# Performance work log

Measured on AMD Instinct MI355X. Metric: run time of the kernel, lower is better.

The kernel has to match this reference:

```python
import jax, jax.numpy as jnp
import numpy as np

N1 = 4096
N2 = 4096


def _encoder(x, w1, b1, w2, b2, w3, b3):
    # fc1 -> fc2 -> fc3 -> relu (relu only after fc3, matching the torch code)
    h = x @ w1.T + b1
    h = h @ w2.T + b2
    h = h @ w3.T + b3
    return jax.nn.relu(h)


def _self_attention(x, adj, alpha, W):
    # tmp_i = sum_j [adj_ij==1] * alpha_ij * W * x_j ; tmp_i /= deg_i ; tmp_i += x_i (only if deg_i != 0)
    a = (adj == 1).astype(x.dtype)          # [N, N]
    deg = a.sum(axis=1)                     # [N]
    agg = (a * alpha) @ x                   # [N, 64] masked weighted aggregation
    agg = agg * W[0, 0]
    safe_deg = jnp.maximum(deg, 1.0)
    out = agg / safe_deg[:, None] + x       # residual
    return jnp.where((deg != 0.0)[:, None], out, jnp.zeros_like(out))


def setup_inputs() -> dict:
    key = jax.random.key(0)
    ks = jax.random.split(key, 20)
    s = 0.02  # weight scale to keep activations sane through the 4096->256->128->64 MLP
    inp = {
        "x1": jax.random.normal(ks[0], (N1, N1), jnp.float32),
        "x2": jax.random.normal(ks[1], (N2, N2), jnp.float32),
        "adj1": jax.random.randint(ks[2], (N1, N1), 0, 2, jnp.int32),
        "adj2": jax.random.randint(ks[3], (N2, N2), 0, 2, jnp.int32),
        "e1_w1": jax.random.normal(ks[4], (256, N1), jnp.float32) * s,
        "e1_b1": jnp.zeros((256,), jnp.float32),
        "e1_w2": jax.random.normal(ks[5], (128, 256), jnp.float32) * s,
        "e1_b2": jnp.zeros((128,), jnp.float32),
        "e1_w3": jax.random.normal(ks[6], (64, 128), jnp.float32) * s,
        "e1_b3": jnp.zeros((64,), jnp.float32),
        "e2_w1": jax.random.normal(ks[7], (256, N2), jnp.float32) * s,
        "e2_b1": jnp.zeros((256,), jnp.float32),
        "e2_w2": jax.random.normal(ks[8], (128, 256), jnp.float32) * s,
        "e2_b2": jnp.zeros((128,), jnp.float32),
        "e2_w3": jax.random.normal(ks[9], (64, 128), jnp.float32) * s,
        "e2_b3": jnp.zeros((64,), jnp.float32),
        "W": jax.random.normal(ks[10], (1, 1), jnp.float32),
        "alpha1": jax.random.normal(ks[11], (N1, N1), jnp.float32),
        "clf_w": jax.random.normal(ks[12], (2, (N1 + N2) * 64), jnp.float32) * s,
        "clf_b": jnp.zeros((2,), jnp.float32),
    }
    return inp


def reference(x1, x2, adj1, adj2,
              e1_w1, e1_b1, e1_w2, e1_b2, e1_w3, e1_b3,
              e2_w1, e2_b1, e2_w2, e2_b2, e2_w3, e2_b3,
              W, alpha1, clf_w, clf_b):
    h1 = _encoder(x1, e1_w1, e1_b1, e1_w2, e1_b2, e1_w3, e1_b3)  # [N1, 64]
    h2 = _encoder(x2, e2_w1, e2_b1, e2_w2, e2_b2, e2_w3, e2_b3)  # [N2, 64]
    # NOTE: original torch code uses self.alpha1 for BOTH graphs (alpha2 is unused)
    new1 = _self_attention(h1, adj1, alpha1, W)
    new2 = _self_attention(h2, adj2, alpha1[:N2, :N2], W)
    feat = jnp.concatenate([new1, new2], axis=0).reshape(1, -1)  # [1, (N1+N2)*64]
    return feat @ clf_w.T + clf_b  # [1, 2]
```

## Files before the change

kernel.cpp:

```cpp
#include <hip/hip_runtime.h>
#include <hip/hip_bf16.h>
#include <stdint.h>

#define N 4096

typedef __attribute__((ext_vector_type(4))) float f32x4;
typedef __attribute__((ext_vector_type(8))) short s16x8;

__device__ inline unsigned short f2bf(float f) {
    unsigned int u = __float_as_uint(f);
    u += 0x7fffu + ((u >> 16) & 1u);
    return (unsigned short)(u >> 16);
}
__device__ inline float bf2f(unsigned short h) {
    return __uint_as_float(((unsigned int)h) << 16);
}

__global__ void k0a(const float* __restrict__ w2a, const float* __restrict__ w3a,
                    const float* __restrict__ b1a, const float* __restrict__ b2a, const float* __restrict__ b3a,
                    const float* __restrict__ w2b, const float* __restrict__ w3b,
                    const float* __restrict__ b1b, const float* __restrict__ b2b, const float* __restrict__ b3b,
                    float* __restrict__ T, float* __restrict__ beff) {
    const int g  = blockIdx.x >> 5;
    const int nb = blockIdx.x & 31;
    const float* w2 = g ? w2b : w2a;
    const float* w3 = g ? w3b : w3a;
    const int c  = threadIdx.x;
    const int n0 = nb * 2;
    float a0 = 0.f, a1 = 0.f;
#pragma unroll 8
    for (int r = 0; r < 128; ++r) {
        float w = w2[r * 256 + c];
        a0 += w3[n0 * 128 + r] * w;
        a1 += w3[n0 * 128 + 128 + r] * w;
    }
    float* Tg = T + g * 64 * 256;
    Tg[n0 * 256 + c]       = a0;
    Tg[(n0 + 1) * 256 + c] = a1;

    if (nb == 0) {
        __shared__ float ps[256];
        __shared__ float u[128];
        const float* b1 = g ? b1b : b1a;
        const float* b2 = g ? b2b : b2a;
        const float* b3 = g ? b3b : b3a;
        {
            const int r = threadIdx.x >> 1, half = threadIdx.x & 1;
            float s = 0.f;
#pragma unroll 8
            for (int cc = 0; cc < 128; ++cc) s += w2[r * 256 + half * 128 + cc] * b1[half * 128 + cc];
            ps[threadIdx.x] = s;
        }
        __syncthreads();
        if (threadIdx.x < 128)
            u[threadIdx.x] = ps[2 * threadIdx.x] + ps[2 * threadIdx.x + 1] + b2[threadIdx.x];
        __syncthreads();
        {
            const int n = threadIdx.x >> 2, qr = threadIdx.x & 3;
            float s = 0.f;
#pragma unroll
            for (int r = 0; r < 32; ++r) s += w3[n * 128 + qr * 32 + r] * u[qr * 32 + r];
            ps[threadIdx.x] = s;
        }
        __syncthreads();
        if (threadIdx.x < 64)
            beff[g * 64 + threadIdx.x] = ps[4 * threadIdx.x] + ps[4 * threadIdx.x + 1]
                                       + ps[4 * threadIdx.x + 2] + ps[4 * threadIdx.x + 3] + b3[threadIdx.x];
    }
}

__global__ __launch_bounds__(256) void k0b(const float* __restrict__ w1a, const float* __restrict__ w1b,
                                           const float* __restrict__ T,
                                           unsigned short* __restrict__ Wfrag) {
    const int b  = blockIdx.x;
    const int g = b >> 8, n4 = (b >> 4) & 15, kchunk = b & 15;
    const float* w1 = g ? w1b : w1a;
    const int kx = kchunk * 256 + threadIdx.x;
    const float* Tg = T + (size_t)(g * 64 + n4 * 4) * 256;
    float acc[4] = {0.f, 0.f, 0.f, 0.f};
#pragma unroll 8
    for (int r = 0; r < 256; ++r) {
        float w = w1[(size_t)r * N + kx];
#pragma unroll
        for (int j = 0; j < 4; ++j) acc[j] += Tg[j * 256 + r] * w;
    }
    const int kc = kx >> 6, cc = (kx >> 5) & 1, q = (kx >> 3) & 3, ko = kx & 7;
#pragma unroll
    for (int j = 0; j < 4; ++j) {
        const int n = n4 * 4 + j;
        const int ng = n >> 4, l15 = n & 15;
        const int lane = q * 16 + l15;
        const unsigned short hi = f2bf(acc[j]);
        const unsigned short lo = f2bf(acc[j] - bf2f(hi));
        const size_t unit = ((((size_t)g * 64 + kc) * 4 + ng) * 2 + cc) * 2;
        Wfrag[unit * 512 + lane * 8 + ko]       = hi;
        Wfrag[(unit + 1) * 512 + lane * 8 + ko] = lo;
    }
}

__global__ __launch_bounds__(512, 2) void k1(const float* __restrict__ x1, const float* __restrict__ x2,
                                             const unsigned short* __restrict__ Wfrag,
                                             float* __restrict__ ph) {
    const int b  = blockIdx.x;
    const int rt = b >> 2, ks = b & 3;
    const int g  = rt >> 6;
    const int rbase = (rt & 63) * 64;
    const float* x = g ? x2 : x1;

    const int t = threadIdx.x;
    const int lane = t & 63, w = t >> 6;
    const int rg = w & 3, kh = w >> 2;
    const int q = lane >> 4, l15 = lane & 15;

    __shared__ float accs_h[4][4][64][4];

    f32x4 acc[4];
#pragma unroll
    for (int ng = 0; ng < 4; ++ng) acc[ng] = (f32x4){0.f, 0.f, 0.f, 0.f};

    const float* xrow = x + (size_t)(rbase + rg * 16 + l15) * N;
    const int kcbase = ks * 16 + kh * 8;

    float4 pa0, pa1, ra0, ra1;
    s16x8 pbh[4], pbl[4], rbh[4], rbl[4];

#define K1_LOAD(A0, A1, BH, BL, IT) do { \
        const int kc_ = kcbase + ((IT) >> 1), c_ = (IT) & 1; \
        const int ka_ = kc_ * 64 + c_ * 32 + q * 8; \
        A0 = *(const float4*)&xrow[ka_]; \
        A1 = *(const float4*)&xrow[ka_ + 4]; \
        _Pragma("unroll") \
        for (int ng = 0; ng < 4; ++ng) { \
            const size_t unit = ((((size_t)g * 64 + kc_) * 4 + ng) * 2 + c_) * 2; \
            BH[ng] = *(const s16x8*)&Wfrag[unit * 512 + lane * 8]; \
            BL[ng] = *(const s16x8*)&Wfrag[(unit + 1) * 512 + lane * 8]; \
        } \
    } while (0)

#define K1_COMP(A0, A1, BH, BL) do { \
        float xv[8] = {A0.x, A0.y, A0.z, A0.w, A1.x, A1.y, A1.z, A1.w}; \
        s16x8 ah, al; \
        _Pragma("unroll") \
        for (int j = 0; j < 8; ++j) { \
            unsigned short hh = f2bf(xv[j]); \
            ah[j] = (short)hh; \
            al[j] = (short)f2bf(xv[j] - bf2f(hh)); \
        } \
        _Pragma("unroll") \
        for (int ng = 0; ng < 4; ++ng) { \
            acc[ng] = __builtin_amdgcn_mfma_f32_16x16x32_bf16(al, BH[ng], acc[ng], 0, 0, 0); \
            acc[ng] = __builtin_amdgcn_mfma_f32_16x16x32_bf16(ah, BL[ng], acc[ng], 0, 0, 0); \
            acc[ng] = __builtin_amdgcn_mfma_f32_16x16x32_bf16(ah, BH[ng], acc[ng], 0, 0, 0); \
        } \
    } while (0)

    K1_LOAD(pa0, pa1, pbh, pbl, 0);
#pragma unroll
    for (int it2 = 0; it2 < 8; ++it2) {
        K1_LOAD(ra0, ra1, rbh, rbl, 2 * it2 + 1);
        K1_COMP(pa0, pa1, pbh, pbl);
        if (it2 < 7) K1_LOAD(pa0, pa1, pbh, pbl, 2 * it2 + 2);
        K1_COMP(ra0, ra1, rbh, rbl);
    }
#undef K1_LOAD
#undef K1_COMP

    if (kh == 1) {
#pragma unroll
        for (int ng = 0; ng < 4; ++ng)
#pragma unroll
            for (int r = 0; r < 4; ++r) accs_h[rg][ng][lane][r] = acc[ng][r];
    }
    __syncthreads();
    if (kh == 0) {
        const int girow = g * 4096 + rbase + rg * 16 + q * 4;
#pragma unroll
        for (int ng = 0; ng < 4; ++ng) {
            const int n = ng * 16 + l15;
#pragma unroll
            for (int r = 0; r < 4; ++r) {
                float s = acc[ng][r] + accs_h[rg][ng][lane][r];
                ph[((size_t)ks * 8192 + girow + r) * 64 + n] = s;
            }
        }
    }
}

__global__ __launch_bounds__(256) void k1b(const float* __restrict__ ph, const float* __restrict__ beff,
                                           float* __restrict__ hf, unsigned short* __restrict__ hfrag) {
    const int b = blockIdx.x;
    const int g = b & 1;
    const int i0 = (b >> 1) * 16;
    const int t = threadIdx.x;
    const int il = t >> 4, nq = t & 15;
    const int gi = g * 4096 + i0 + il;

    __shared__ unsigned short htile[64][16];

    f32x4 s = (f32x4){0.f, 0.f, 0.f, 0.f};
#pragma unroll
    for (int ks = 0; ks < 4; ++ks)
        s += *(const f32x4*)&ph[((size_t)ks * 8192 + gi) * 64 + nq * 4];
    f32x4 o;
#pragma unroll
    for (int j = 0; j < 4; ++j) {
        const int n = nq * 4 + j;
        float v = fmaxf(s[j] + beff[g * 64 + n], 0.f);
        o[j] = v;
        htile[n][il] = f2bf(v);
    }
    *(f32x4*)&hf[(size_t)gi * 64 + nq * 4] = o;
    __syncthreads();

    if (t < 128) {
        const int ng2 = t >> 5, jh = (t >> 4) & 1, l = t & 15;
        uint4 v = *(const uint4*)&htile[ng2 * 16 + l][jh * 8];
        const int jc = i0 >> 6, c = (i0 >> 5) & 1, q0 = (i0 >> 3) & 3;
        const size_t unit = (((size_t)g * 4 + ng2) * 64 + jc) * 2 + c;
        *(uint4*)&hfrag[unit * 512 + (size_t)(q0 + jh) * 128 + l * 8] = v;
    }
}

__global__ __launch_bounds__(512, 2) void k2(const int* __restrict__ adj1, const int* __restrict__ adj2,
                                             const float* __restrict__ alpha,
                                             const unsigned short* __restrict__ hfrag,
                                             float* __restrict__ pagg, float* __restrict__ pdeg) {
    const int b  = blockIdx.x;
    const int ks = (b >> 1) & 3;
    const int i0 = ((((b >> 3) << 1) | (b & 1))) << 4;
    const int t = threadIdx.x;
    const int lane = t & 63, kg = t >> 6;
    const int q = lane >> 4, l15 = lane & 15;

    __shared__ __align__(16) unsigned short am[2][2][16][256];
    __shared__ float degp[2][16][32];
    float (*accs)[4][64][4] = reinterpret_cast<float (*)[4][64][4]>(&am[0][0][0][0]);

    f32x4 acc1[4], acc2[4];
#pragma unroll
    for (int ng = 0; ng < 4; ++ng) {
        acc1[ng] = (f32x4){0.f, 0.f, 0.f, 0.f};
        acc2[ng] = (f32x4){0.f, 0.f, 0.f, 0.f};
    }
    int deg1 = 0, deg2 = 0;

    const int srow = t >> 5, scg = t & 31;
    const size_t sbase = (size_t)(i0 + srow) * N + (size_t)ks * 1024 + (size_t)scg * 8;
    char* const amb = (char*)&am[0][0][0][0];
    const int swoff = (srow * 512 + scg * 16) ^ ((srow & 7) << 4);
    const int rdoff = (l15 * 512 + kg * 64 + q * 16) ^ ((l15 & 7) << 4);

    float4 sa0, sa1; int4 sj10, sj11, sj20, sj21;

#define K2_ISSUE(S) do { \
        const float* ap = alpha + sbase + (S) * 256; \
        sa0 = *(const float4*)ap; sa1 = *(const float4*)(ap + 4); \
        const int* p1 = adj1 + sbase + (S) * 256; \
        sj10 = *(const int4*)p1; sj11 = *(const int4*)(p1 + 4); \
        const int* p2 = adj2 + sbase + (S) * 256; \
        sj20 = *(const int4*)p2; sj21 = *(const int4*)(p2 + 4); \
    } while (0)

#define K2_CONVSTORE(BUF) do { \
        float av[8] = {sa0.x, sa0.y, sa0.z, sa0.w, sa1.x, sa1.y, sa1.z, sa1.w}; \
        int m1[8] = {sj10.x == 1, sj10.y == 1, sj10.z == 1, sj10.w == 1, \
                     sj11.x == 1, sj11.y == 1, sj11.z == 1, sj11.w == 1}; \
        int m2[8] = {sj20.x == 1, sj20.y == 1, sj20.z == 1, sj20.w == 1, \
                     sj21.x == 1, sj21.y == 1, sj21.z == 1, sj21.w == 1}; \
        s16x8 w1v, w2v; \
        _Pragma("unroll") \
        for (int j = 0; j < 8; ++j) { \
            unsigned short bv = f2bf(av[j]); \
            w1v[j] = m1[j] ? (short)bv : (short)0; \
            w2v[j] = m2[j] ? (short)bv : (short)0; \
            deg1 += m1[j]; deg2 += m2[j]; \
        } \
        *(s16x8*)(amb + (BUF) * 16384 + swoff) = w1v; \
        *(s16x8*)(amb + (BUF) * 16384 + 8192 + swoff) = w2v; \
    } while (0)

#define K2_COMPUTE(S) do { \
        const int jc = ks * 16 + (S) * 4 + (kg >> 1), cph = kg & 1; \
        s16x8 ha1[4], ha2[4]; \
        _Pragma("unroll") \
        for (int ng = 0; ng < 4; ++ng) { \
            const size_t u1 = (((size_t)ng) * 64 + jc) * 2 + cph; \
            const size_t u2 = (((size_t)(4 + ng)) * 64 + jc) * 2 + cph; \
            ha1[ng] = *(const s16x8*)&hfrag[u1 * 512 + lane * 8]; \
            ha2[ng] = *(const s16x8*)&hfrag[u2 * 512 + lane * 8]; \
        } \
        s16x8 bfa = *(const s16x8*)(amb + ((S) & 1) * 16384 + rdoff); \
        s16x8 bfb = *(const s16x8*)(amb + ((S) & 1) * 16384 + 8192 + rdoff); \
        _Pragma("unroll") \
        for (int ng = 0; ng < 4; ++ng) { \
            acc1[ng] = __builtin_amdgcn_mfma_f32_16x16x32_bf16(ha1[ng], bfa, acc1[ng], 0, 0, 0); \
            acc2[ng] = __builtin_amdgcn_mfma_f32_16x16x32_bf16(ha2[ng], bfb, acc2[ng], 0, 0, 0); \
        } \
    } while (0)

    K2_ISSUE(0);
    K2_CONVSTORE(0);
    __syncthreads();
#pragma unroll
    for (int s = 0; s < 4; ++s) {
        if (s < 3) K2_ISSUE(s + 1);
        K2_COMPUTE(s);
        if (s < 3) K2_CONVSTORE((s + 1) & 1);
        __syncthreads();
    }

    degp[0][srow][scg] = (float)deg1;
    degp[1][srow][scg] = (float)deg2;
#pragma unroll
    for (int ng = 0; ng < 4; ++ng)
#pragma unroll
        for (int r = 0; r < 4; ++r) accs[kg][ng][lane][r] = acc1[ng][r];
    __syncthreads();
    if (t < 32) {
        const int gg = t >> 4, row = t & 15;
        float s = 0.f;
#pragma unroll
        for (int c2 = 0; c2 < 32; ++c2) s += degp[gg][row][c2];
        pdeg[(size_t)(gg * 4 + ks) * 4096 + i0 + row] = s;
    }

    {
        const int ng = kg & 3, rh = kg >> 2;
        const int i = i0 + l15;
#pragma unroll
        for (int rr = 0; rr < 2; ++rr) {
            const int r = rh * 2 + rr;
            float s = 0.f;
#pragma unroll
            for (int k8 = 0; k8 < 8; ++k8) s += accs[k8][ng][lane][r];
            const int n = ng * 16 + q * 4 + r;
            pagg[(((size_t)ks * 4096 + i) << 6) + n] = s;
        }
    }
    __syncthreads();
#pragma unroll
    for (int ng = 0; ng < 4; ++ng)
#pragma unroll
        for (int r = 0; r < 4; ++r) accs[kg][ng][lane][r] = acc2[ng][r];
    __syncthreads();
    {
        const int ng = kg & 3, rh = kg >> 2;
        const int i = i0 + l15;
#pragma unroll
        for (int rr = 0; rr < 2; ++rr) {
            const int r = rh * 2 + rr;
            float s = 0.f;
#pragma unroll
            for (int k8 = 0; k8 < 8; ++k8) s += accs[k8][ng][lane][r];
            const int n = ng * 16 + q * 4 + r;
            pagg[(((size_t)(4 + ks) * 4096 + i) << 6) + n] = s;
        }
    }
#undef K2_ISSUE
#undef K2_CONVSTORE
#undef K2_COMPUTE
}

__global__ __launch_bounds__(256) void k2b(const float* __restrict__ pagg, const float* __restrict__ pdeg,
                                           const float* __restrict__ hf, const float* __restrict__ Wp,
                                           float* __restrict__ outv) {
    const int idx = blockIdx.x * 256 + threadIdx.x;
    const int gi  = idx >> 4;
    const int nq  = idx & 15;
    const int g   = gi >> 12, i = gi & 4095;
    const float W00 = Wp[0];

    float dg = 0.f;
#pragma unroll
    for (int ks = 0; ks < 4; ++ks) dg += pdeg[(size_t)(g * 4 + ks) * 4096 + i];

    f32x4 s = (f32x4){0.f, 0.f, 0.f, 0.f};
#pragma unroll
    for (int ks = 0; ks < 4; ++ks) {
        const f32x4 p = *(const f32x4*)&pagg[(((size_t)(g * 4 + ks) * 4096 + i) << 6) + nq * 4];
        s += p;
    }
    const f32x4 hv = *(const f32x4*)&hf[((size_t)gi << 6) + nq * 4];
    const float dmax = fmaxf(dg, 1.f);
    f32x4 o;
#pragma unroll
    for (int j = 0; j < 4; ++j)
        o[j] = (dg != 0.f) ? (s[j] * W00 / dmax + hv[j]) : 0.f;
    *(f32x4*)&outv[((size_t)gi << 6) + nq * 4] = o;
}

__global__ __launch_bounds__(256) void k3a(const float* __restrict__ feat, const float* __restrict__ clfw,
                                           float* __restrict__ part) {
    const int t = threadIdx.x;
    const size_t idx = (size_t)blockIdx.x * 2048 + (size_t)t * 8;
    float4 a0 = *(const float4*)&feat[idx];
    float4 a1 = *(const float4*)&feat[idx + 4];
    float4 c0 = *(const float4*)&clfw[idx];
    float4 c1 = *(const float4*)&clfw[idx + 4];
    float4 d0 = *(const float4*)&clfw[524288 + idx];
    float4 d1 = *(const float4*)&clfw[524288 + idx + 4];
    float s0 = a0.x * c0.x + a0.y * c0.y + a0.z * c0.z + a0.w * c0.w
             + a1.x * c1.x + a1.y * c1.y + a1.z * c1.z + a1.w * c1.w;
    float s1 = a0.x * d0.x + a0.y * d0.y + a0.z * d0.z + a0.w * d0.w
             + a1.x * d1.x + a1.y * d1.y + a1.z * d1.z + a1.w * d1.w;
    __shared__ float r0[256], r1[256];
    r0[t] = s0; r1[t] = s1;
    __syncthreads();
    for (int s = 128; s > 0; s >>= 1) {
        if (t < s) { r0[t] += r0[t + s]; r1[t] += r1[t + s]; }
        __syncthreads();
    }
    if (t == 0) { part[blockIdx.x * 2] = r0[0]; part[blockIdx.x * 2 + 1] = r1[0]; }
}

__global__ void k3b(const float* __restrict__ part, const float* __restrict__ clfb,
                    float* __restrict__ outp) {
    const int t = threadIdx.x;
    __shared__ float r0[256], r1[256];
    r0[t] = part[t * 2]; r1[t] = part[t * 2 + 1];
    __syncthreads();
    for (int s = 128; s > 0; s >>= 1) {
        if (t < s) { r0[t] += r0[t + s]; r1[t] += r1[t + s]; }
        __syncthreads();
    }
    if (t == 0) { outp[0] = r0[0] + clfb[0]; outp[1] = r1[0] + clfb[1]; }
}

extern "C" void kernel_launch(void* const* d_in, const int* in_sizes, int n_in,
                              void* d_out, int out_size, void* d_ws, size_t ws_size,
                              hipStream_t stream) {
    const float* x1   = (const float*)d_in[0];
    const float* x2   = (const float*)d_in[1];
    const int*   adj1 = (const int*)d_in[2];
    const int*   adj2 = (const int*)d_in[3];
    const float* e1w1 = (const float*)d_in[4];
    const float* e1b1 = (const float*)d_in[5];
    const float* e1w2 = (const float*)d_in[6];
    const float* e1b2 = (const float*)d_in[7];
    const float* e1w3 = (const float*)d_in[8];
    const float* e1b3 = (const float*)d_in[9];
    const float* e2w1 = (const float*)d_in[10];
    const float* e2b1 = (const float*)d_in[11];
    const float* e2w2 = (const float*)d_in[12];
    const float* e2b2 = (const float*)d_in[13];
    const float* e2w3 = (const float*)d_in[14];
    const float* e2b3 = (const float*)d_in[15];
    const float* Wp   = (const float*)d_in[16];
    const float* alph = (const float*)d_in[17];
    const float* clfw = (const float*)d_in[18];
    const float* clfb = (const float*)d_in[19];

    char* wsb = (char*)d_ws;
    unsigned short* Wfrag = (unsigned short*)(wsb);
    float* newv = (float*)(wsb);
    unsigned short* hfrag = (unsigned short*)(wsb + (2u << 20));
    float* hf   = (float*)(wsb + (3u << 20));
    float* T    = (float*)(wsb + (5u << 20));
    float* beff = (float*)(wsb + (5u << 20) + (1u << 17));
    float* part = (float*)(wsb + (5u << 20) + (1u << 17) + 4096);
    float* pagg = (float*)(wsb + (6u << 20));
    float* ph   = (float*)(wsb + (6u << 20));
    float* pdeg = (float*)(wsb + (14u << 20));

    hipLaunchKernelGGL(k0a, dim3(64), dim3(256), 0, stream,
                       e1w2, e1w3, e1b1, e1b2, e1b3, e2w2, e2w3, e2b1, e2b2, e2b3, T, beff);
    hipLaunchKernelGGL(k0b, dim3(512), dim3(256), 0, stream, e1w1, e2w1, T, Wfrag);
    hipLaunchKernelGGL(k1, dim3(512), dim3(512), 0, stream, x1, x2, Wfrag, ph);
    hipLaunchKernelGGL(k1b, dim3(512), dim3(256), 0, stream, ph, beff, hf, hfrag);
    hipLaunchKernelGGL(k2, dim3(1024), dim3(512), 0, stream, adj1, adj2, alph, hfrag, pagg, pdeg);
    hipLaunchKernelGGL(k2b, dim3(512), dim3(256), 0, stream, pagg, pdeg, hf, Wp, newv);
    hipLaunchKernelGGL(k3a, dim3(256), dim3(256), 0, stream, newv, clfw, part);
    hipLaunchKernelGGL(k3b, dim3(1), dim3(256), 0, stream, part, clfb, (float*)d_out);
}
```

Baseline: 393.5 us.

## Deepen prefetch in aggregation kernel and restructure MLP fragment loads with sched barriers

In the fc1 GEMM kernel, weight fragments are now loaded just before use inside each step. Only the x activations are prefetched, and the steps are separated by sched_barrier, which should lower register pressure and keep the compiler from reordering. In the aggregation kernel, alpha/adj global loads are prefetched two stages ahead into two register sets. The full __syncthreads is replaced by an LDS-only waitcnt plus s_barrier, so more global loads stay in flight while the MFMAs run. This costs extra VGPRs for the second prefetch set, and the hand-placed scheduling barriers may limit compiler interleaving.

New measurement: 391.6 us. Within noise of the previous version (-0.5%).

```diff
diff --git a/kernel.cpp b/kernel.cpp
--- a/kernel.cpp
+++ b/kernel.cpp
@@ -122,22 +122,23 @@
     const int kcbase = ks * 16 + kh * 8;
 
     float4 pa0, pa1, ra0, ra1;
-    s16x8 pbh[4], pbl[4], rbh[4], rbl[4];
-
-#define K1_LOAD(A0, A1, BH, BL, IT) do { \
+
+#define K1_LOADX(A0, A1, IT) do { \
         const int kc_ = kcbase + ((IT) >> 1), c_ = (IT) & 1; \
         const int ka_ = kc_ * 64 + c_ * 32 + q * 8; \
         A0 = *(const float4*)&xrow[ka_]; \
         A1 = *(const float4*)&xrow[ka_ + 4]; \
+    } while (0)
+
+#define K1_STEP(A0, A1, IT) do { \
+        const int kc_ = kcbase + ((IT) >> 1), c_ = (IT) & 1; \
+        s16x8 bh[4], bl[4]; \
         _Pragma("unroll") \
         for (int ng = 0; ng < 4; ++ng) { \
             const size_t unit = ((((size_t)g * 64 + kc_) * 4 + ng) * 2 + c_) * 2; \
-            BH[ng] = *(const s16x8*)&Wfrag[unit * 512 + lane * 8]; \
-            BL[ng] = *(const s16x8*)&Wfrag[(unit + 1) * 512 + lane * 8]; \
-        } \
-    } while (0)
-
-#define K1_COMP(A0, A1, BH, BL) do { \
+            bh[ng] = *(const s16x8*)&Wfrag[unit * 512 + lane * 8]; \
+            bl[ng] = *(const s16x8*)&Wfrag[(unit + 1) * 512 + lane * 8]; \
+        } \
         float xv[8] = {A0.x, A0.y, A0.z, A0.w, A1.x, A1.y, A1.z, A1.w}; \
         s16x8 ah, al; \
         _Pragma("unroll") \
@@ -148,22 +149,27 @@
         } \
         _Pragma("unroll") \
         for (int ng = 0; ng < 4; ++ng) { \
-            acc[ng] = __builtin_amdgcn_mfma_f32_16x16x32_bf16(al, BH[ng], acc[ng], 0, 0, 0); \
-            acc[ng] = __builtin_amdgcn_mfma_f32_16x16x32_bf16(ah, BL[ng], acc[ng], 0, 0, 0); \
-            acc[ng] = __builtin_amdgcn_mfma_f32_16x16x32_bf16(ah, BH[ng], acc[ng], 0, 0, 0); \
-        } \
-    } while (0)
-
-    K1_LOAD(pa0, pa1, pbh, pbl, 0);
+            acc[ng] = __builtin_amdgcn_mfma_f32_16x16x32_bf16(al, bh[ng], acc[ng], 0, 0, 0); \
+            acc[ng] = __builtin_amdgcn_mfma_f32_16x16x32_bf16(ah, bl[ng], acc[ng], 0, 0, 0); \
+            acc[ng] = __builtin_amdgcn_mfma_f32_16x16x32_bf16(ah, bh[ng], acc[ng], 0, 0, 0); \
+        } \
+    } while (0)
+
+    K1_LOADX(pa0, pa1, 0);
+    __builtin_amdgcn_sched_barrier(0);
 #pragma unroll
     for (int it2 = 0; it2 < 8; ++it2) {
-        K1_LOAD(ra0, ra1, rbh, rbl, 2 * it2 + 1);
-        K1_COMP(pa0, pa1, pbh, pbl);
-        if (it2 < 7) K1_LOAD(pa0, pa1, pbh, pbl, 2 * it2 + 2);
-        K1_COMP(ra0, ra1, rbh, rbl);
-    }
-#undef K1_LOAD
-#undef K1_COMP
+        K1_LOADX(ra0, ra1, 2 * it2 + 1);
+        __builtin_amdgcn_sched_barrier(0);
+        K1_STEP(pa0, pa1, 2 * it2);
+        if (it2 < 7) {
+            K1_LOADX(pa0, pa1, 2 * it2 + 2);
+            __builtin_amdgcn_sched_barrier(0);
+        }
+        K1_STEP(ra0, ra1, 2 * it2 + 1);
+    }
+#undef K1_LOADX
+#undef K1_STEP
 
     if (kh == 1) {
 #pragma unroll
@@ -250,23 +256,24 @@
     const int swoff = (srow * 512 + scg * 16) ^ ((srow & 7) << 4);
     const int rdoff = (l15 * 512 + kg * 64 + q * 16) ^ ((l15 & 7) << 4);
 
-    float4 sa0, sa1; int4 sj10, sj11, sj20, sj21;
-
-#define K2_ISSUE(S) do { \
-        const float* ap = alpha + sbase + (S) * 256; \
-        sa0 = *(const float4*)ap; sa1 = *(const float4*)(ap + 4); \
-        const int* p1 = adj1 + sbase + (S) * 256; \
-        sj10 = *(const int4*)p1; sj11 = *(const int4*)(p1 + 4); \
-        const int* p2 = adj2 + sbase + (S) * 256; \
-        sj20 = *(const int4*)p2; sj21 = *(const int4*)(p2 + 4); \
-    } while (0)
-
-#define K2_CONVSTORE(BUF) do { \
-        float av[8] = {sa0.x, sa0.y, sa0.z, sa0.w, sa1.x, sa1.y, sa1.z, sa1.w}; \
-        int m1[8] = {sj10.x == 1, sj10.y == 1, sj10.z == 1, sj10.w == 1, \
-                     sj11.x == 1, sj11.y == 1, sj11.z == 1, sj11.w == 1}; \
-        int m2[8] = {sj20.x == 1, sj20.y == 1, sj20.z == 1, sj20.w == 1, \
-                     sj21.x == 1, sj21.y == 1, sj21.z == 1, sj21.w == 1}; \
+    float4 saA0, saA1, saB0, saB1;
+    int4 sjA10, sjA11, sjA20, sjA21, sjB10, sjB11, sjB20, sjB21;
+
+#define K2_ISSUE(P0, P1, J10, J11, J20, J21, S) do { \
+        const float* ap_ = alpha + sbase + (S) * 256; \
+        P0 = *(const float4*)ap_; P1 = *(const float4*)(ap_ + 4); \
+        const int* p1_ = adj1 + sbase + (S) * 256; \
+        J10 = *(const int4*)p1_; J11 = *(const int4*)(p1_ + 4); \
+        const int* p2_ = adj2 + sbase + (S) * 256; \
+        J20 = *(const int4*)p2_; J21 = *(const int4*)(p2_ + 4); \
+    } while (0)
+
+#define K2_CONV(P0, P1, J10, J11, J20, J21, BUF) do { \
+        float av[8] = {P0.x, P0.y, P0.z, P0.w, P1.x, P1.y, P1.z, P1.w}; \
+        int m1[8] = {J10.x == 1, J10.y == 1, J10.z == 1, J10.w == 1, \
+                     J11.x == 1, J11.y == 1, J11.z == 1, J11.w == 1}; \
+        int m2[8] = {J20.x == 1, J20.y == 1, J20.z == 1, J20.w == 1, \
+                     J21.x == 1, J21.y == 1, J21.z == 1, J21.w == 1}; \
         s16x8 w1v, w2v; \
         _Pragma("unroll") \
         for (int j = 0; j < 8; ++j) { \
@@ -279,7 +286,7 @@
         *(s16x8*)(amb + (BUF) * 16384 + 8192 + swoff) = w2v; \
     } while (0)
 
-#define K2_COMPUTE(S) do { \
+#define K2_COMPUTE(S, BUF) do { \
         const int jc = ks * 16 + (S) * 4 + (kg >> 1), cph = kg & 1; \
         s16x8 ha1[4], ha2[4]; \
         _Pragma("unroll") \
@@ -289,8 +296,8 @@
             ha1[ng] = *(const s16x8*)&hfrag[u1 * 512 + lane * 8]; \
             ha2[ng] = *(const s16x8*)&hfrag[u2 * 512 + lane * 8]; \
         } \
-        s16x8 bfa = *(const s16x8*)(amb + ((S) & 1) * 16384 + rdoff); \
-        s16x8 bfb = *(const s16x8*)(amb + ((S) & 1) * 16384 + 8192 + rdoff); \
+        s16x8 bfa = *(const s16x8*)(amb + (BUF) * 16384 + rdoff); \
+        s16x8 bfb = *(const s16x8*)(amb + (BUF) * 16384 + 8192 + rdoff); \
         _Pragma("unroll") \
         for (int ng = 0; ng < 4; ++ng) { \
             acc1[ng] = __builtin_amdgcn_mfma_f32_16x16x32_bf16(ha1[ng], bfa, acc1[ng], 0, 0, 0); \
@@ -298,16 +305,29 @@
         } \
     } while (0)
 
-    K2_ISSUE(0);
-    K2_CONVSTORE(0);
-    __syncthreads();
-#pragma unroll
-    for (int s = 0; s < 4; ++s) {
-        if (s < 3) K2_ISSUE(s + 1);
-        K2_COMPUTE(s);
-        if (s < 3) K2_CONVSTORE((s + 1) & 1);
-        __syncthreads();
-    }
+#define K2_FENCE() do { \
+        __builtin_amdgcn_sched_barrier(0); \
+        asm volatile("s_waitcnt lgkmcnt(0)" ::: "memory"); \
+        __builtin_amdgcn_s_barrier(); \
+    } while (0)
+
+    K2_ISSUE(saA0, saA1, sjA10, sjA11, sjA20, sjA21, 0);
+    K2_ISSUE(saB0, saB1, sjB10, sjB11, sjB20, sjB21, 1);
+    K2_CONV (saA0, saA1, sjA10, sjA11, sjA20, sjA21, 0);
+    K2_ISSUE(saA0, saA1, sjA10, sjA11, sjA20, sjA21, 2);
+    K2_FENCE();
+    K2_COMPUTE(0, 0);
+    K2_CONV (saB0, saB1, sjB10, sjB11, sjB20, sjB21, 1);
+    K2_ISSUE(saB0, saB1, sjB10, sjB11, sjB20, sjB21, 3);
+    K2_FENCE();
+    K2_COMPUTE(1, 1);
+    K2_CONV (saA0, saA1, sjA10, sjA11, sjA20, sjA21, 0);
+    K2_FENCE();
+    K2_COMPUTE(2, 0);
+    K2_CONV (saB0, saB1, sjB10, sjB11, sjB20, sjB21, 1);
+    K2_FENCE();
+    K2_COMPUTE(3, 1);
+    __syncthreads();
 
     degp[0][srow][scg] = (float)deg1;
     degp[1][srow][scg] = (float)deg2;
@@ -357,8 +377,9 @@
         }
     }
 #undef K2_ISSUE
-#undef K2_CONVSTORE
+#undef K2_CONV
 #undef K2_COMPUTE
+#undef K2_FENCE
 }
 
 __global__ __launch_bounds__(256) void k2b(const float* __restrict__ pagg, const float* __restrict__ pdeg,
```

## Stage x tiles through swizzled LDS with coalesced loads in k1

Applied to the files above, without the earlier changes.

The fc1 GEMM kernel now loads x rows with wide, coalesced float4 reads into registers, splits them into bf16 hi/lo once, and stores them into an XOR-swizzled LDS tile. MFMA warps then read A fragments from LDS, with the two warp halves covering interleaved k-chunks within each staged slab. The goal is better global-memory coalescing for the dominant 2x64MB x read and no duplicated conversion work. In exchange it adds LDS traffic, two barriers per stage, and drops the previous register double-buffering that overlapped loads with MFMA.

Measured after the change: 401.7 us. 2.1% more time.

```diff
diff --git a/kernel.cpp b/kernel.cpp
--- a/kernel.cpp
+++ b/kernel.cpp
@@ -109,70 +109,81 @@
 
     const int t = threadIdx.x;
     const int lane = t & 63, w = t >> 6;
-    const int rg = w & 3, kh = w >> 2;
+    const int rg = w & 3, ch = w >> 2;
     const int q = lane >> 4, l15 = lane & 15;
 
-    __shared__ float accs_h[4][4][64][4];
+    __shared__ __align__(16) unsigned short amx[2][64][256];
+    char* const amb = (char*)&amx[0][0][0];
+    float (*accs_h)[4][64][4] = reinterpret_cast<float (*)[4][64][4]>(amb);
 
     f32x4 acc[4];
 #pragma unroll
     for (int ng = 0; ng < 4; ++ng) acc[ng] = (f32x4){0.f, 0.f, 0.f, 0.f};
 
-    const float* xrow = x + (size_t)(rbase + rg * 16 + l15) * N;
-    const int kcbase = ks * 16 + kh * 8;
-
-    float4 pa0, pa1, ra0, ra1;
-    s16x8 pbh[4], pbl[4], rbh[4], rbl[4];
-
-#define K1_LOAD(A0, A1, BH, BL, IT) do { \
-        const int kc_ = kcbase + ((IT) >> 1), c_ = (IT) & 1; \
-        const int ka_ = kc_ * 64 + c_ * 32 + q * 8; \
-        A0 = *(const float4*)&xrow[ka_]; \
-        A1 = *(const float4*)&xrow[ka_ + 4]; \
-        _Pragma("unroll") \
-        for (int ng = 0; ng < 4; ++ng) { \
-            const size_t unit = ((((size_t)g * 64 + kc_) * 4 + ng) * 2 + c_) * 2; \
-            BH[ng] = *(const s16x8*)&Wfrag[unit * 512 + lane * 8]; \
-            BL[ng] = *(const s16x8*)&Wfrag[(unit + 1) * 512 + lane * 8]; \
-        } \
-    } while (0)
-
-#define K1_COMP(A0, A1, BH, BL) do { \
-        float xv[8] = {A0.x, A0.y, A0.z, A0.w, A1.x, A1.y, A1.z, A1.w}; \
-        s16x8 ah, al; \
-        _Pragma("unroll") \
-        for (int j = 0; j < 8; ++j) { \
-            unsigned short hh = f2bf(xv[j]); \
-            ah[j] = (short)hh; \
-            al[j] = (short)f2bf(xv[j] - bf2f(hh)); \
-        } \
-        _Pragma("unroll") \
-        for (int ng = 0; ng < 4; ++ng) { \
-            acc[ng] = __builtin_amdgcn_mfma_f32_16x16x32_bf16(al, BH[ng], acc[ng], 0, 0, 0); \
-            acc[ng] = __builtin_amdgcn_mfma_f32_16x16x32_bf16(ah, BL[ng], acc[ng], 0, 0, 0); \
-            acc[ng] = __builtin_amdgcn_mfma_f32_16x16x32_bf16(ah, BH[ng], acc[ng], 0, 0, 0); \
-        } \
-    } while (0)
-
-    K1_LOAD(pa0, pa1, pbh, pbl, 0);
-#pragma unroll
-    for (int it2 = 0; it2 < 8; ++it2) {
-        K1_LOAD(ra0, ra1, rbh, rbl, 2 * it2 + 1);
-        K1_COMP(pa0, pa1, pbh, pbl);
-        if (it2 < 7) K1_LOAD(pa0, pa1, pbh, pbl, 2 * it2 + 2);
-        K1_COMP(ra0, ra1, rbh, rbl);
-    }
-#undef K1_LOAD
-#undef K1_COMP
-
-    if (kh == 1) {
+    const int srow = t >> 3, scol = (t & 7) * 32;
+    const float* xs = x + (size_t)(rbase + srow) * N + ks * 1024 + scol;
+    const int swz = (srow & 7) << 4;
+
+    const int rdrow = rg * 16 + l15;
+    const int rswz = (rdrow & 7) << 4;
+
+    for (int s = 0; s < 4; ++s) {
+        float4 xv4[8];
+#pragma unroll
+        for (int u = 0; u < 8; ++u) xv4[u] = *(const float4*)&xs[s * 256 + u * 4];
+#pragma unroll
+        for (int u2 = 0; u2 < 4; ++u2) {
+            const float4 a = xv4[2 * u2], b2 = xv4[2 * u2 + 1];
+            const float fv[8] = {a.x, a.y, a.z, a.w, b2.x, b2.y, b2.z, b2.w};
+            s16x8 hi8, lo8;
+#pragma unroll
+            for (int j = 0; j < 8; ++j) {
+                const unsigned short h = f2bf(fv[j]);
+                hi8[j] = (short)h;
+                lo8[j] = (short)f2bf(fv[j] - bf2f(h));
+            }
+            const int boff = (srow * 512 + (scol + u2 * 8) * 2) ^ swz;
+            *(s16x8*)(amb + boff)         = hi8;
+            *(s16x8*)(amb + 32768 + boff) = lo8;
+        }
+        __syncthreads();
+
+#pragma unroll
+        for (int kk = 0; kk < 2; ++kk) {
+            const int kcl = ch * 2 + kk;
+            const int kc  = ks * 16 + s * 4 + kcl;
+#pragma unroll
+            for (int c = 0; c < 2; ++c) {
+                const int col = kcl * 64 + c * 32 + q * 8;
+                const int ro  = (rdrow * 512 + col * 2) ^ rswz;
+                s16x8 ah = *(const s16x8*)(amb + ro);
+                s16x8 al = *(const s16x8*)(amb + 32768 + ro);
+                s16x8 bh[4], bl[4];
+#pragma unroll
+                for (int ng = 0; ng < 4; ++ng) {
+                    const size_t unit = ((((size_t)g * 64 + kc) * 4 + ng) * 2 + c) * 2;
+                    bh[ng] = *(const s16x8*)&Wfrag[unit * 512 + lane * 8];
+                    bl[ng] = *(const s16x8*)&Wfrag[(unit + 1) * 512 + lane * 8];
+                }
+#pragma unroll
+                for (int ng = 0; ng < 4; ++ng) {
+                    acc[ng] = __builtin_amdgcn_mfma_f32_16x16x32_bf16(al, bh[ng], acc[ng], 0, 0, 0);
+                    acc[ng] = __builtin_amdgcn_mfma_f32_16x16x32_bf16(ah, bl[ng], acc[ng], 0, 0, 0);
+                    acc[ng] = __builtin_amdgcn_mfma_f32_16x16x32_bf16(ah, bh[ng], acc[ng], 0, 0, 0);
+                }
+            }
+        }
+        __syncthreads();
+    }
+
+    if (ch == 1) {
 #pragma unroll
         for (int ng = 0; ng < 4; ++ng)
 #pragma unroll
             for (int r = 0; r < 4; ++r) accs_h[rg][ng][lane][r] = acc[ng][r];
     }
     __syncthreads();
-    if (kh == 0) {
+    if (ch == 0) {
         const int girow = g * 4096 + rbase + rg * 16 + q * 4;
 #pragma unroll
         for (int ng = 0; ng < 4; ++ng) {
```
